# Kernel optimization log

Measured on AMD Instinct MI355X. Metric: run time of the kernel, lower is better.

The kernel has to match this reference:

```python
import jax, jax.numpy as jnp
import numpy as np

B, T, E = 16, 1024, 1024
G, N, D = 4, 8, 128
V = 2048


def setup_inputs() -> dict:
    key = jax.random.key(0)
    k1, k2, k3, k4 = jax.random.split(key, 4)
    x_emb = jax.random.normal(k1, (B, T, E), dtype=jnp.float32)
    W_in = jax.random.normal(k2, (E, G * N * D), dtype=jnp.float32) / np.sqrt(E)
    R = jax.random.normal(k3, (G, N, D, D), dtype=jnp.float32) / np.sqrt(D)
    b = jnp.zeros((G, N, D), dtype=jnp.float32)
    W_proj = jax.random.normal(k4, (V, N * D), dtype=jnp.float32) / np.sqrt(D)
    b_proj = jnp.zeros((V,), dtype=jnp.float32)
    return {"x_emb": x_emb, "W_in": W_in, "R": R, "b": b, "W_proj": W_proj, "b_proj": b_proj}


def reference(x_emb, W_in, R, b, W_proj, b_proj):
    # Input projection for all timesteps at once: [B,T,G,N,D]
    Bx, Tx, Ex = x_emb.shape
    Wx = jnp.einsum('bte,eg->btg', x_emb, W_in).reshape(Bx, Tx, G, N, D)

    def step(carry, wx_t):
        h, c = carry  # [B,N,D] each
        # per-head matrix recurrence: R[g] @ h  -> [B,G,N,D]
        gates = wx_t + jnp.einsum('gnde,bne->bgnd', R, h) + b
        i = jax.nn.sigmoid(gates[:, 0])
        f = jax.nn.sigmoid(gates[:, 1])
        z = jnp.tanh(gates[:, 2])
        o = jax.nn.sigmoid(gates[:, 3])
        c_new = f * c + i * z
        h_new = o * jnp.tanh(c_new)
        return (h_new, c_new), h_new

    h0 = jnp.zeros((Bx, N, D), dtype=x_emb.dtype)
    c0 = jnp.zeros((Bx, N, D), dtype=x_emb.dtype)
    (hN, cN), hs = jax.lax.scan(step, (h0, c0), jnp.swapaxes(Wx, 0, 1))  # hs: [T,B,N,D]
    h_flat = jnp.swapaxes(hs, 0, 1).reshape(Bx, Tx, N * D)
    logits = jnp.einsum('btn,vn->btv', h_flat, W_proj) + b_proj
    return logits
```

## Files before the change

### kernel.cpp

```cpp
#include <hip/hip_runtime.h>
#include <hip/hip_bf16.h>

#define DEV __device__ __forceinline__

using bf16 = __hip_bfloat16;
typedef __attribute__((ext_vector_type(8))) short short8v;
typedef __attribute__((ext_vector_type(4))) float f32x4;

constexpr int Bq = 16, Tq = 1024, Eq = 1024, Gq = 4, Nq = 8, Dq = 128, Vq = 2048;
constexpr int M1 = Bq * Tq;
constexpr int N1q = Gq * Nq * Dq;
constexpr int K1 = Eq;
constexpr int K2 = Nq * Dq;
constexpr int N2 = Vq;

DEV unsigned short bfu(float x) {
  union { bf16 h; unsigned short u; } cv;
  cv.h = __float2bfloat16(x);
  return cv.u;
}

DEV float rcp_(float x) { return __builtin_amdgcn_rcpf(x); }
DEV float sigm(float x) { return rcp_(1.0f + __expf(-x)); }
DEV float tanh_(float x) { return fmaf(2.0f, rcp_(1.0f + __expf(-2.0f * x)), -1.0f); }

#define GLD16(gp, lp)                                                       \
  __builtin_amdgcn_global_load_lds(                                        \
      (const __attribute__((address_space(1))) void*)(gp),                 \
      (__attribute__((address_space(3))) void*)(lp), 16, 0, 0)

#define SBAR0() __builtin_amdgcn_sched_barrier(0)
#define RAWBAR()                                                            \
  do { SBAR0(); __builtin_amdgcn_s_barrier(); SBAR0(); } while (0)
#define VMW6() asm volatile("s_waitcnt vmcnt(6)" ::: "memory")
#define VMW3() asm volatile("s_waitcnt vmcnt(3)" ::: "memory")
#define VMW0() asm volatile("s_waitcnt vmcnt(0)" ::: "memory")

__global__ __launch_bounds__(256) void cast_f32_bf16(const float* __restrict__ s,
                                                     bf16* __restrict__ d, int n4) {
  const int i = blockIdx.x * 256 + threadIdx.x;
  if (i >= n4) return;
  const float4 v = ((const float4*)s)[i];
  ushort4 u;
  u.x = bfu(v.x); u.y = bfu(v.y); u.z = bfu(v.z); u.w = bfu(v.w);
  ((ushort4*)d)[i] = u;
}

__global__ __launch_bounds__(256) void transpose_cast_perm(const float* __restrict__ s,
                                                           bf16* __restrict__ d,
                                                           int SK, int SN) {
  __shared__ float t[32][33];
  const int n0 = blockIdx.x * 32, k0 = blockIdx.y * 32;
  const int tx = threadIdx.x & 31, ty = threadIdx.x >> 5;
#pragma unroll
  for (int i = 0; i < 32; i += 8)
    t[ty + i][tx] = s[(size_t)(k0 + ty + i) * SN + n0 + tx];
  __syncthreads();
#pragma unroll
  for (int i = 0; i < 32; i += 8) {
    const int c = n0 + ty + i;
    const int g = c >> 10, n = (c >> 7) & 7, dd = c & 127;
    const int rp = n * 512 + dd * 4 + g;
    d[(size_t)rp * SK + k0 + tx] = __float2bfloat16(t[tx][ty + i]);
  }
}

__global__ __launch_bounds__(256) void zero_flags(unsigned int* __restrict__ f) {
  f[blockIdx.x * 256 + threadIdx.x] = 0u;
}

__global__ __launch_bounds__(256) void gemm_out(const bf16* __restrict__ A,
                                                const bf16* __restrict__ Bt,
                                                float* __restrict__ C,
                                                const float* __restrict__ bp,
                                                int K, int N) {
  __shared__ bf16 As[128 * 32];
  __shared__ bf16 Bs[128 * 32];
  const int m0 = blockIdx.y * 128, n0 = blockIdx.x * 128;
  const int tid = threadIdx.x;
  const int lane = tid & 63, w = tid >> 6;
  const int wm = w >> 1, wn = w & 1;

  const int srow = lane >> 2, scol = (lane & 3) * 8;
  const int ca = w * 2;
  const bf16* Ag0 = A + (size_t)(m0 + ca * 16 + srow) * K + scol;
  const bf16* Ag1 = Ag0 + (size_t)16 * K;
  const bf16* Bg0 = Bt + (size_t)(n0 + ca * 16 + srow) * K + scol;
  const bf16* Bg1 = Bg0 + (size_t)16 * K;
  bf16* Al0 = As + ca * 512;
  bf16* Al1 = Al0 + 512;
  bf16* Bl0 = Bs + ca * 512;
  bf16* Bl1 = Bl0 + 512;

  f32x4 acc[4][4] = {};
  const int rr = lane & 15;
  const int kb = (lane >> 4) * 8;

  for (int k0 = 0; k0 < K; k0 += 32) {
    GLD16(Ag0 + k0, Al0);
    GLD16(Ag1 + k0, Al1);
    GLD16(Bg0 + k0, Bl0);
    GLD16(Bg1 + k0, Bl1);
    __syncthreads();
    short8v af[4], bfr[4];
#pragma unroll
    for (int i = 0; i < 4; ++i) {
      af[i]  = *(const short8v*)&As[(wm * 64 + i * 16 + rr) * 32 + kb];
      bfr[i] = *(const short8v*)&Bs[(wn * 64 + i * 16 + rr) * 32 + kb];
    }
#pragma unroll
    for (int i = 0; i < 4; ++i)
#pragma unroll
      for (int j = 0; j < 4; ++j)
        acc[i][j] = __builtin_amdgcn_mfma_f32_16x16x32_bf16(af[i], bfr[j], acc[i][j], 0, 0, 0);
    __syncthreads();
  }

  const int crow = (lane >> 4) * 4, ccol = lane & 15;
  float bv[4];
#pragma unroll
  for (int j = 0; j < 4; ++j) bv[j] = bp[n0 + wn * 64 + j * 16 + ccol];
#pragma unroll
  for (int i = 0; i < 4; ++i)
#pragma unroll
    for (int j = 0; j < 4; ++j) {
      const size_t base =
          (size_t)(m0 + wm * 64 + i * 16 + crow) * N + (n0 + wn * 64 + j * 16 + ccol);
#pragma unroll
      for (int jj = 0; jj < 4; ++jj)
        C[base + (size_t)jj * N] = acc[i][j][jj] + bv[j];
    }
}

__global__ __launch_bounds__(512) void fused_xw_lstm(
    const bf16* __restrict__ xb, const bf16* __restrict__ WiT,
    bf16* __restrict__ Wx, const float* __restrict__ bp,
    const float* __restrict__ R, bf16* __restrict__ h_all,
    unsigned int* flags) {
  __shared__ bf16 Ab[4][128 * 32];
  __shared__ bf16 Bb[4][2][128 * 32];
  __shared__ __align__(16) unsigned short hl[2][4][144];

  const int bid = blockIdx.x;
  const int tid = threadIdx.x;

  if (bid < 224) {
    const int lane = tid & 63;
    const int w8 = tid >> 6;
    const int ts = w8 >> 2;
    const int w4 = w8 & 3;
    const int wm = w4 >> 1, wn = w4 & 1;
    const int rr = lane & 15, kb = (lane >> 4) * 8;
    const int crow = (lane >> 4) * 4, ccol = lane & 15;
    const int frow = 16 * w8 + (lane >> 2);
    const int fcol = (lane & 3) * 8;
    bf16* const Adst = &Ab[0][16 * w8 * 32];
    bf16* const B0dst = &Bb[0][0][16 * w8 * 32];
    bf16* const B1dst = &Bb[0][1][16 * w8 * 32];

    for (int pi = bid; pi < 2048; pi += 224) {
      const int tix0 = pi * 2;
      const int s = tix0 >> 9;
      const int rem = tix0 & 511;
      const int bn = rem >> 2, q0 = rem & 3;
      const int b = bn >> 3, n = bn & 7;
      const int m0 = (b * 8 + s) * 128;
      const int n0base = (n * 4 + q0) * 128;

      const bf16* Asrc = xb + (size_t)(m0 + frow) * 1024 + fcol;
      const bf16* B0src = WiT + (size_t)(n0base + frow) * 1024 + fcol;
      const bf16* B1src = B0src + (size_t)128 * 1024;

#define FILLCHUNK(BUF, KC)                                                   \
  do {                                                                       \
    const size_t go_ = (size_t)(KC) * 32;                                    \
    GLD16(Asrc + go_, Adst + (BUF) * 4096);                                  \
    GLD16(B0src + go_, B0dst + (BUF) * 8192);                                \
    GLD16(B1src + go_, B1dst + (BUF) * 8192);                                \
  } while (0)

      f32x4 acc[4][4] = {};

#define COMPUTECHUNK(BUF)                                                    \
  do {                                                                       \
    const bf16* Ap_ = &Ab[(BUF)][0];                                         \
    const bf16* Bp_ = &Bb[(BUF)][ts][0];                                     \
    short8v af[4], bfr[4];                                                   \
    _Pragma("unroll") for (int i2 = 0; i2 < 4; ++i2) {                       \
      af[i2]  = *(const short8v*)&Ap_[(wm * 64 + i2 * 16 + rr) * 32 + kb];   \
      bfr[i2] = *(const short8v*)&Bp_[(wn * 64 + i2 * 16 + rr) * 32 + kb];   \
    }                                                                        \
    _Pragma("unroll") for (int i2 = 0; i2 < 4; ++i2)                         \
      _Pragma("unroll") for (int j2 = 0; j2 < 4; ++j2)                       \
        acc[i2][j2] = __builtin_amdgcn_mfma_f32_16x16x32_bf16(               \
            af[i2], bfr[j2], acc[i2][j2], 0, 0, 0);                          \
  } while (0)

      FILLCHUNK(0, 0);
      FILLCHUNK(1, 1);
      for (int i = 0; i < 30; ++i) {
        FILLCHUNK((i + 2) & 3, i + 2);
        VMW6();
        RAWBAR();
        COMPUTECHUNK(i & 3);
      }
      VMW3();
      RAWBAR();
      COMPUTECHUNK(2);
      VMW0();
      RAWBAR();
      COMPUTECHUNK(3);

      {
        const int n0t = n0base + ts * 128;
#pragma unroll
        for (int i = 0; i < 4; ++i)
#pragma unroll
          for (int j = 0; j < 4; ++j) {
            const int pc = n0t + wn * 64 + j * 16 + ccol;
            const int nn = pc >> 9, gd = pc & 511;
            const int g = gd & 3, dd = gd >> 2;
            const float bvj = bp[(g * 8 + nn) * 128 + dd];
#pragma unroll
            for (int jj = 0; jj < 4; ++jj) {
              const int row = m0 + wm * 64 + i * 16 + crow + jj;
              const int bb = row >> 10, t = row & 1023;
              const size_t idx = (((size_t)(bb * 8 + nn) << 10) + t) * 512 + gd;
              Wx[idx] = __float2bfloat16(acc[i][j][jj] + bvj);
            }
          }
      }
      __syncthreads();
      if (tid == 0) {
        __threadfence();
        __hip_atomic_fetch_add(&flags[bn * 8 + s], 2u,
                               __ATOMIC_RELEASE, __HIP_MEMORY_SCOPE_AGENT);
      }
    }
#undef FILLCHUNK
#undef COMPUTECHUNK
  } else {
    const int cid = bid - 224;
    const int n = cid & 7, bq = cid >> 3;
    const int w = tid >> 6, lane = tid & 63;
    const int lg = lane >> 4, lc = lane & 15;
    const int bloc = lc & 3;
    const int ci = lc >> 2;
    const int dsite = 16 * w + 4 * ci + lg;

    short8v Af[4][4];
#pragma unroll
    for (int tau = 0; tau < 4; ++tau) {
      const int gd = 64 * w + 16 * tau + lc;
      const int g = gd & 3, d = gd >> 2;
      const float* rbase = R + ((size_t)(g * 8 + n) * 128 + d) * 128;
#pragma unroll
      for (int kf = 0; kf < 4; ++kf) {
        const float* rp = rbase + 32 * kf + 8 * lg;
        const float4 r0 = *(const float4*)rp;
        const float4 r1 = *(const float4*)(rp + 4);
        short8v bv;
        bv[0] = (short)bfu(r0.x); bv[1] = (short)bfu(r0.y);
        bv[2] = (short)bfu(r0.z); bv[3] = (short)bfu(r0.w);
        bv[4] = (short)bfu(r1.x); bv[5] = (short)bfu(r1.y);
        bv[6] = (short)bfu(r1.z); bv[7] = (short)bfu(r1.w);
        Af[tau][kf] = bv;
      }
    }

    for (int i = tid; i < 4 * 144; i += 512) (&hl[0][0][0])[i] = 0;
    __syncthreads();

    const bf16* wxb =
        Wx + ((size_t)((bq * 4 + bloc) * 8 + n) << 10) * 512 + dsite * 4;
    bf16* hout = h_all + ((size_t)(bq * 4 + bloc) << 20) + n * 128 + dsite;

    float c = 0.f;

    for (int s = 0; s < 8; ++s) {
      if (tid == 0) {
#pragma unroll
        for (int j = 0; j < 4; ++j) {
          const int fidx = ((bq * 4 + j) * 8 + n) * 8 + s;
          while (__hip_atomic_load(&flags[fidx], __ATOMIC_RELAXED,
                                   __HIP_MEMORY_SCOPE_AGENT) < 4u)
            __builtin_amdgcn_s_sleep(2);
        }
        __threadfence();
      }
      __syncthreads();

      ushort4 wxr[4];
#pragma unroll
      for (int u = 0; u < 4; ++u)
        wxr[u] = *(const ushort4*)(wxb + (size_t)(s * 128 + u) * 512);

      const int tend = s * 128 + 128;
      for (int t0 = s * 128; t0 < tend; t0 += 4) {
#pragma unroll
        for (int u = 0; u < 4; ++u) {
          const int t = t0 + u;
          const unsigned short* hb = &hl[t & 1][0][0];
          short8v Bf[4];
#pragma unroll
          for (int kf = 0; kf < 4; ++kf)
            Bf[kf] = *(const short8v*)(hb + bloc * 144 + kf * 32 + lg * 8);

          const ushort4 wxc = wxr[u];

          f32x4 acc[4];
#pragma unroll
          for (int tau = 0; tau < 4; ++tau) {
            acc[tau][0] = 0.f; acc[tau][1] = 0.f;
            acc[tau][2] = 0.f; acc[tau][3] = 0.f;
          }
#pragma unroll
          for (int kf = 0; kf < 4; ++kf)
#pragma unroll
            for (int tau = 0; tau < 4; ++tau)
              acc[tau] = __builtin_amdgcn_mfma_f32_16x16x32_bf16(
                  Af[tau][kf], Bf[kf], acc[tau], 0, 0, 0);

          {
            const int tp = (t + 4 < tend) ? (t + 4) : (tend - 1);
            wxr[u] = *(const ushort4*)(wxb + (size_t)tp * 512);
          }

          float pre0 = (ci & 2) ? ((ci & 1) ? acc[3][0] : acc[2][0])
                                : ((ci & 1) ? acc[1][0] : acc[0][0]);
          float pre1 = (ci & 2) ? ((ci & 1) ? acc[3][1] : acc[2][1])
                                : ((ci & 1) ? acc[1][1] : acc[0][1]);
          float pre2 = (ci & 2) ? ((ci & 1) ? acc[3][2] : acc[2][2])
                                : ((ci & 1) ? acc[1][2] : acc[0][2]);
          float pre3 = (ci & 2) ? ((ci & 1) ? acc[3][3] : acc[2][3])
                                : ((ci & 1) ? acc[1][3] : acc[0][3]);
          pre0 += __uint_as_float((unsigned)wxc.x << 16);
          pre1 += __uint_as_float((unsigned)wxc.y << 16);
          pre2 += __uint_as_float((unsigned)wxc.z << 16);
          pre3 += __uint_as_float((unsigned)wxc.w << 16);

          const float i_ = sigm(pre0);
          const float f_ = sigm(pre1);
          const float z_ = tanh_(pre2);
          const float o_ = sigm(pre3);
          c = f_ * c + i_ * z_;
          const float h = o_ * tanh_(c);
          const bf16 h16 = __float2bfloat16(h);

          hl[(t + 1) & 1][bloc][dsite] = ((const unsigned short*)&h16)[0];
          hout[(size_t)t << 10] = h16;

          __builtin_amdgcn_sched_barrier(0);
          asm volatile("s_waitcnt lgkmcnt(0)" ::: "memory");
          __builtin_amdgcn_sched_barrier(0);
          __builtin_amdgcn_s_barrier();
          __builtin_amdgcn_sched_barrier(0);
        }
      }
    }
  }
}

extern "C" void kernel_launch(void* const* d_in, const int* in_sizes, int n_in,
                              void* d_out, int out_size, void* d_ws, size_t ws_size,
                              hipStream_t stream) {
  const float* x_emb = (const float*)d_in[0];
  const float* W_in  = (const float*)d_in[1];
  const float* R     = (const float*)d_in[2];
  const float* bias  = (const float*)d_in[3];
  const float* W_prj = (const float*)d_in[4];
  const float* b_prj = (const float*)d_in[5];

  char* ws = (char*)d_ws;
  bf16* xb  = (bf16*)ws;
  bf16* WiT = (bf16*)(ws + (size_t)M1 * K1 * 2);
  bf16* Wpb = WiT + (size_t)N1q * K1;
  bf16* H   = Wpb + (size_t)N2 * K2;
  unsigned int* flags = (unsigned int*)(ws + ((size_t)76 << 20));
  bf16* Wx = (bf16*)d_out;

  cast_f32_bf16<<<(M1 * K1 / 4 + 255) / 256, 256, 0, stream>>>(x_emb, xb, M1 * K1 / 4);
  transpose_cast_perm<<<dim3(N1q / 32, K1 / 32), 256, 0, stream>>>(W_in, WiT, K1, N1q);
  cast_f32_bf16<<<(N2 * K2 / 4 + 255) / 256, 256, 0, stream>>>(W_prj, Wpb, N2 * K2 / 4);
  zero_flags<<<4, 256, 0, stream>>>(flags);

  fused_xw_lstm<<<dim3(256), dim3(512), 0, stream>>>(xb, WiT, Wx, bias, R, H, flags);

  gemm_out<<<dim3(N2 / 128, M1 / 128), 256, 0, stream>>>(
      H, Wpb, (float*)d_out, b_prj, K2, N2);
}
```

Baseline: 767.8 us.

## Fuse output projection into persistent LSTM kernel with per-chunk h flags

Moves the final vocabulary projection GEMM into the persistent fused kernel. The 224 GEMM blocks, once they finish the input projection, wait on new per-(batch, time-chunk) flags that the recurrence blocks publish. They then compute logits tiles while the serial recurrence keeps running. The Wx scratch in the output buffer is re-laid out so each (batch, chunk) slice lines up with the logits rows that later overwrite it, which keeps the in-place reuse safe. The cost is a second launch traded for spin-waiting. The projection GEMM now uses only 224 blocks with a smaller 128x128 tile per 8-wave block, so it may run below full-device throughput after the recurrence ends.

Result: slower. 793.9 us (+3.4%).

```diff
diff --git a/kernel.cpp b/kernel.cpp
--- a/kernel.cpp
+++ b/kernel.cpp
@@ -69,74 +69,12 @@
   f[blockIdx.x * 256 + threadIdx.x] = 0u;
 }
 
-__global__ __launch_bounds__(256) void gemm_out(const bf16* __restrict__ A,
-                                                const bf16* __restrict__ Bt,
-                                                float* __restrict__ C,
-                                                const float* __restrict__ bp,
-                                                int K, int N) {
-  __shared__ bf16 As[128 * 32];
-  __shared__ bf16 Bs[128 * 32];
-  const int m0 = blockIdx.y * 128, n0 = blockIdx.x * 128;
-  const int tid = threadIdx.x;
-  const int lane = tid & 63, w = tid >> 6;
-  const int wm = w >> 1, wn = w & 1;
-
-  const int srow = lane >> 2, scol = (lane & 3) * 8;
-  const int ca = w * 2;
-  const bf16* Ag0 = A + (size_t)(m0 + ca * 16 + srow) * K + scol;
-  const bf16* Ag1 = Ag0 + (size_t)16 * K;
-  const bf16* Bg0 = Bt + (size_t)(n0 + ca * 16 + srow) * K + scol;
-  const bf16* Bg1 = Bg0 + (size_t)16 * K;
-  bf16* Al0 = As + ca * 512;
-  bf16* Al1 = Al0 + 512;
-  bf16* Bl0 = Bs + ca * 512;
-  bf16* Bl1 = Bl0 + 512;
-
-  f32x4 acc[4][4] = {};
-  const int rr = lane & 15;
-  const int kb = (lane >> 4) * 8;
-
-  for (int k0 = 0; k0 < K; k0 += 32) {
-    GLD16(Ag0 + k0, Al0);
-    GLD16(Ag1 + k0, Al1);
-    GLD16(Bg0 + k0, Bl0);
-    GLD16(Bg1 + k0, Bl1);
-    __syncthreads();
-    short8v af[4], bfr[4];
-#pragma unroll
-    for (int i = 0; i < 4; ++i) {
-      af[i]  = *(const short8v*)&As[(wm * 64 + i * 16 + rr) * 32 + kb];
-      bfr[i] = *(const short8v*)&Bs[(wn * 64 + i * 16 + rr) * 32 + kb];
-    }
-#pragma unroll
-    for (int i = 0; i < 4; ++i)
-#pragma unroll
-      for (int j = 0; j < 4; ++j)
-        acc[i][j] = __builtin_amdgcn_mfma_f32_16x16x32_bf16(af[i], bfr[j], acc[i][j], 0, 0, 0);
-    __syncthreads();
-  }
-
-  const int crow = (lane >> 4) * 4, ccol = lane & 15;
-  float bv[4];
-#pragma unroll
-  for (int j = 0; j < 4; ++j) bv[j] = bp[n0 + wn * 64 + j * 16 + ccol];
-#pragma unroll
-  for (int i = 0; i < 4; ++i)
-#pragma unroll
-    for (int j = 0; j < 4; ++j) {
-      const size_t base =
-          (size_t)(m0 + wm * 64 + i * 16 + crow) * N + (n0 + wn * 64 + j * 16 + ccol);
-#pragma unroll
-      for (int jj = 0; jj < 4; ++jj)
-        C[base + (size_t)jj * N] = acc[i][j][jj] + bv[j];
-    }
-}
-
-__global__ __launch_bounds__(512) void fused_xw_lstm(
+__global__ __launch_bounds__(512) void fused_all(
     const bf16* __restrict__ xb, const bf16* __restrict__ WiT,
-    bf16* __restrict__ Wx, const float* __restrict__ bp,
+    bf16* __restrict__ WxC, const float* __restrict__ bp,
     const float* __restrict__ R, bf16* __restrict__ h_all,
-    unsigned int* flags) {
+    const bf16* __restrict__ Wpb, const float* __restrict__ bprj,
+    float* __restrict__ out, unsigned int* wxflags, unsigned int* hflags) {
   __shared__ bf16 Ab[4][128 * 32];
   __shared__ bf16 Bb[4][2][128 * 32];
   __shared__ __align__(16) unsigned short hl[2][4][144];
@@ -147,29 +85,30 @@
   if (bid < 224) {
     const int lane = tid & 63;
     const int w8 = tid >> 6;
-    const int ts = w8 >> 2;
-    const int w4 = w8 & 3;
-    const int wm = w4 >> 1, wn = w4 & 1;
-    const int rr = lane & 15, kb = (lane >> 4) * 8;
-    const int crow = (lane >> 4) * 4, ccol = lane & 15;
-    const int frow = 16 * w8 + (lane >> 2);
-    const int fcol = (lane & 3) * 8;
-    bf16* const Adst = &Ab[0][16 * w8 * 32];
-    bf16* const B0dst = &Bb[0][0][16 * w8 * 32];
-    bf16* const B1dst = &Bb[0][1][16 * w8 * 32];
-
-    for (int pi = bid; pi < 2048; pi += 224) {
-      const int tix0 = pi * 2;
-      const int s = tix0 >> 9;
-      const int rem = tix0 & 511;
-      const int bn = rem >> 2, q0 = rem & 3;
-      const int b = bn >> 3, n = bn & 7;
-      const int m0 = (b * 8 + s) * 128;
-      const int n0base = (n * 4 + q0) * 128;
-
-      const bf16* Asrc = xb + (size_t)(m0 + frow) * 1024 + fcol;
-      const bf16* B0src = WiT + (size_t)(n0base + frow) * 1024 + fcol;
-      const bf16* B1src = B0src + (size_t)128 * 1024;
+    {
+      const int ts = w8 >> 2;
+      const int w4 = w8 & 3;
+      const int wm = w4 >> 1, wn = w4 & 1;
+      const int rr = lane & 15, kb = (lane >> 4) * 8;
+      const int crow = (lane >> 4) * 4, ccol = lane & 15;
+      const int frow = 16 * w8 + (lane >> 2);
+      const int fcol = (lane & 3) * 8;
+      bf16* const Adst = &Ab[0][16 * w8 * 32];
+      bf16* const B0dst = &Bb[0][0][16 * w8 * 32];
+      bf16* const B1dst = &Bb[0][1][16 * w8 * 32];
+
+      for (int pi = bid; pi < 2048; pi += 224) {
+        const int tix0 = pi * 2;
+        const int s = tix0 >> 9;
+        const int rem = tix0 & 511;
+        const int bn = rem >> 2, q0 = rem & 3;
+        const int b = bn >> 3, n = bn & 7;
+        const int m0 = (b * 8 + s) * 128;
+        const int n0base = (n * 4 + q0) * 128;
+
+        const bf16* Asrc = xb + (size_t)(m0 + frow) * 1024 + fcol;
+        const bf16* B0src = WiT + (size_t)(n0base + frow) * 1024 + fcol;
+        const bf16* B1src = B0src + (size_t)128 * 1024;
 
 #define FILLCHUNK(BUF, KC)                                                   \
   do {                                                                       \
@@ -179,7 +118,7 @@
     GLD16(B1src + go_, B1dst + (BUF) * 8192);                                \
   } while (0)
 
-      f32x4 acc[4][4] = {};
+        f32x4 acc[4][4] = {};
 
 #define COMPUTECHUNK(BUF)                                                    \
   do {                                                                       \
@@ -196,49 +135,114 @@
             af[i2], bfr[j2], acc[i2][j2], 0, 0, 0);                          \
   } while (0)
 
-      FILLCHUNK(0, 0);
-      FILLCHUNK(1, 1);
-      for (int i = 0; i < 30; ++i) {
-        FILLCHUNK((i + 2) & 3, i + 2);
-        VMW6();
+        FILLCHUNK(0, 0);
+        FILLCHUNK(1, 1);
+        for (int i = 0; i < 30; ++i) {
+          FILLCHUNK((i + 2) & 3, i + 2);
+          VMW6();
+          RAWBAR();
+          COMPUTECHUNK(i & 3);
+        }
+        VMW3();
         RAWBAR();
-        COMPUTECHUNK(i & 3);
-      }
-      VMW3();
-      RAWBAR();
-      COMPUTECHUNK(2);
-      VMW0();
-      RAWBAR();
-      COMPUTECHUNK(3);
-
-      {
-        const int n0t = n0base + ts * 128;
-#pragma unroll
-        for (int i = 0; i < 4; ++i)
-#pragma unroll
-          for (int j = 0; j < 4; ++j) {
-            const int pc = n0t + wn * 64 + j * 16 + ccol;
-            const int nn = pc >> 9, gd = pc & 511;
-            const int g = gd & 3, dd = gd >> 2;
-            const float bvj = bp[(g * 8 + nn) * 128 + dd];
-#pragma unroll
-            for (int jj = 0; jj < 4; ++jj) {
-              const int row = m0 + wm * 64 + i * 16 + crow + jj;
-              const int bb = row >> 10, t = row & 1023;
-              const size_t idx = (((size_t)(bb * 8 + nn) << 10) + t) * 512 + gd;
-              Wx[idx] = __float2bfloat16(acc[i][j][jj] + bvj);
+        COMPUTECHUNK(2);
+        VMW0();
+        RAWBAR();
+        COMPUTECHUNK(3);
+
+        {
+          const int n0t = n0base + ts * 128;
+#pragma unroll
+          for (int i = 0; i < 4; ++i)
+#pragma unroll
+            for (int j = 0; j < 4; ++j) {
+              const int pc = n0t + wn * 64 + j * 16 + ccol;
+              const int nn = pc >> 9, gd = pc & 511;
+              const int g = gd & 3, dd = gd >> 2;
+              const float bvj = bp[(g * 8 + nn) * 128 + dd];
+#pragma unroll
+              for (int jj = 0; jj < 4; ++jj) {
+                const int row = m0 + wm * 64 + i * 16 + crow + jj;
+                const int bb = row >> 10, ss = (row >> 7) & 7, tau = row & 127;
+                const size_t idx = ((size_t)bb << 22) + ((size_t)ss << 19) +
+                                   ((size_t)(nn * 128 + tau) << 9) + gd;
+                WxC[idx] = __float2bfloat16(acc[i][j][jj] + bvj);
+              }
             }
-          }
-      }
-      __syncthreads();
-      if (tid == 0) {
-        __threadfence();
-        __hip_atomic_fetch_add(&flags[bn * 8 + s], 2u,
-                               __ATOMIC_RELEASE, __HIP_MEMORY_SCOPE_AGENT);
-      }
-    }
+        }
+        __syncthreads();
+        if (tid == 0) {
+          __threadfence();
+          __hip_atomic_fetch_add(&wxflags[bn * 8 + s], 2u,
+                                 __ATOMIC_RELEASE, __HIP_MEMORY_SCOPE_AGENT);
+        }
+      }
 #undef FILLCHUNK
 #undef COMPUTECHUNK
+    }
+    {
+      bf16* const AsO = &Ab[0][0];
+      bf16* const BsO = &Ab[1][0];
+      const int wm2 = w8 >> 2, wn2 = w8 & 3;
+      const int srow = lane >> 2, scol = (lane & 3) * 8;
+      const int rr = lane & 15, kb = (lane >> 4) * 8;
+      const int crow = (lane >> 4) * 4, ccol = lane & 15;
+      __syncthreads();
+
+      for (int oi = bid; oi < 2048; oi += 224) {
+        const int so = oi >> 8;
+        const int rem = oi & 255;
+        const int bo = rem >> 4, nc = rem & 15;
+        const int m0 = bo * 1024 + so * 128;
+        const int n0 = nc * 128;
+
+        if (tid == 0) {
+          while (__hip_atomic_load(&hflags[bo * 8 + so], __ATOMIC_RELAXED,
+                                   __HIP_MEMORY_SCOPE_AGENT) < 8u)
+            __builtin_amdgcn_s_sleep(16);
+          __threadfence();
+        }
+        __syncthreads();
+
+        f32x4 acc[4][2] = {};
+        const bf16* Ag = h_all + (size_t)(m0 + 16 * w8 + srow) * 1024 + scol;
+        const bf16* Bg = Wpb + (size_t)(n0 + 16 * w8 + srow) * 1024 + scol;
+        for (int k0 = 0; k0 < 1024; k0 += 32) {
+          GLD16(Ag + k0, AsO + w8 * 512);
+          GLD16(Bg + k0, BsO + w8 * 512);
+          __syncthreads();
+          short8v af[4], bfr[2];
+#pragma unroll
+          for (int i = 0; i < 4; ++i)
+            af[i] = *(const short8v*)&AsO[(wm2 * 64 + i * 16 + rr) * 32 + kb];
+#pragma unroll
+          for (int j = 0; j < 2; ++j)
+            bfr[j] = *(const short8v*)&BsO[(wn2 * 32 + j * 16 + rr) * 32 + kb];
+#pragma unroll
+          for (int i = 0; i < 4; ++i)
+#pragma unroll
+            for (int j = 0; j < 2; ++j)
+              acc[i][j] = __builtin_amdgcn_mfma_f32_16x16x32_bf16(
+                  af[i], bfr[j], acc[i][j], 0, 0, 0);
+          __syncthreads();
+        }
+        float bv[2];
+#pragma unroll
+        for (int j = 0; j < 2; ++j) bv[j] = bprj[n0 + wn2 * 32 + j * 16 + ccol];
+#pragma unroll
+        for (int i = 0; i < 4; ++i)
+#pragma unroll
+          for (int j = 0; j < 2; ++j) {
+            const size_t base =
+                (size_t)(m0 + wm2 * 64 + i * 16 + crow) * N2 +
+                (n0 + wn2 * 32 + j * 16 + ccol);
+#pragma unroll
+            for (int jj = 0; jj < 4; ++jj)
+              out[base + (size_t)jj * N2] = acc[i][j][jj] + bv[j];
+          }
+        __syncthreads();
+      }
+    }
   } else {
     const int cid = bid - 224;
     const int n = cid & 7, bq = cid >> 3;
@@ -247,6 +251,7 @@
     const int bloc = lc & 3;
     const int ci = lc >> 2;
     const int dsite = 16 * w + 4 * ci + lg;
+    const int b = bq * 4 + bloc;
 
     short8v Af[4][4];
 #pragma unroll
@@ -271,10 +276,7 @@
     for (int i = tid; i < 4 * 144; i += 512) (&hl[0][0][0])[i] = 0;
     __syncthreads();
 
-    const bf16* wxb =
-        Wx + ((size_t)((bq * 4 + bloc) * 8 + n) << 10) * 512 + dsite * 4;
-    bf16* hout = h_all + ((size_t)(bq * 4 + bloc) << 20) + n * 128 + dsite;
-
+    bf16* hout = h_all + ((size_t)b << 20) + n * 128 + dsite;
     float c = 0.f;
 
     for (int s = 0; s < 8; ++s) {
@@ -282,7 +284,7 @@
 #pragma unroll
         for (int j = 0; j < 4; ++j) {
           const int fidx = ((bq * 4 + j) * 8 + n) * 8 + s;
-          while (__hip_atomic_load(&flags[fidx], __ATOMIC_RELAXED,
+          while (__hip_atomic_load(&wxflags[fidx], __ATOMIC_RELAXED,
                                    __HIP_MEMORY_SCOPE_AGENT) < 4u)
             __builtin_amdgcn_s_sleep(2);
         }
@@ -290,16 +292,19 @@
       }
       __syncthreads();
 
+      const bf16* wxs = WxC + ((size_t)b << 22) + ((size_t)s << 19) +
+                        ((size_t)(n * 128) << 9) + dsite * 4;
+
       ushort4 wxr[4];
 #pragma unroll
       for (int u = 0; u < 4; ++u)
-        wxr[u] = *(const ushort4*)(wxb + (size_t)(s * 128 + u) * 512);
-
-      const int tend = s * 128 + 128;
-      for (int t0 = s * 128; t0 < tend; t0 += 4) {
+        wxr[u] = *(const ushort4*)(wxs + (size_t)u * 512);
+
+      for (int tau0 = 0; tau0 < 128; tau0 += 4) {
 #pragma unroll
         for (int u = 0; u < 4; ++u) {
-          const int t = t0 + u;
+          const int tau = tau0 + u;
+          const int t = s * 128 + tau;
           const unsigned short* hb = &hl[t & 1][0][0];
           short8v Bf[4];
 #pragma unroll
@@ -310,20 +315,20 @@
 
           f32x4 acc[4];
 #pragma unroll
-          for (int tau = 0; tau < 4; ++tau) {
-            acc[tau][0] = 0.f; acc[tau][1] = 0.f;
-            acc[tau][2] = 0.f; acc[tau][3] = 0.f;
+          for (int tt = 0; tt < 4; ++tt) {
+            acc[tt][0] = 0.f; acc[tt][1] = 0.f;
+            acc[tt][2] = 0.f; acc[tt][3] = 0.f;
           }
 #pragma unroll
           for (int kf = 0; kf < 4; ++kf)
 #pragma unroll
-            for (int tau = 0; tau < 4; ++tau)
-              acc[tau] = __builtin_amdgcn_mfma_f32_16x16x32_bf16(
-                  Af[tau][kf], Bf[kf], acc[tau], 0, 0, 0);
+            for (int tt = 0; tt < 4; ++tt)
+              acc[tt] = __builtin_amdgcn_mfma_f32_16x16x32_bf16(
+                  Af[tt][kf], Bf[kf], acc[tt], 0, 0, 0);
 
           {
-            const int tp = (t + 4 < tend) ? (t + 4) : (tend - 1);
-            wxr[u] = *(const ushort4*)(wxb + (size_t)tp * 512);
+            const int tp = (tau + 4 < 128) ? (tau + 4) : 127;
+            wxr[u] = *(const ushort4*)(wxs + (size_t)tp * 512);
           }
 
           float pre0 = (ci & 2) ? ((ci & 1) ? acc[3][0] : acc[2][0])
@@ -357,6 +362,15 @@
           __builtin_amdgcn_sched_barrier(0);
         }
       }
+
+      __syncthreads();
+      if (tid == 0) {
+        __threadfence();
+#pragma unroll
+        for (int j = 0; j < 4; ++j)
+          __hip_atomic_fetch_add(&hflags[(bq * 4 + j) * 8 + s], 1u,
+                                 __ATOMIC_RELEASE, __HIP_MEMORY_SCOPE_AGENT);
+      }
     }
   }
 }
@@ -377,15 +391,15 @@
   bf16* Wpb = WiT + (size_t)N1q * K1;
   bf16* H   = Wpb + (size_t)N2 * K2;
   unsigned int* flags = (unsigned int*)(ws + ((size_t)76 << 20));
+  unsigned int* wxflags = flags;
+  unsigned int* hflags  = flags + 1024;
   bf16* Wx = (bf16*)d_out;
 
   cast_f32_bf16<<<(M1 * K1 / 4 + 255) / 256, 256, 0, stream>>>(x_emb, xb, M1 * K1 / 4);
   transpose_cast_perm<<<dim3(N1q / 32, K1 / 32), 256, 0, stream>>>(W_in, WiT, K1, N1q);
   cast_f32_bf16<<<(N2 * K2 / 4 + 255) / 256, 256, 0, stream>>>(W_prj, Wpb, N2 * K2 / 4);
-  zero_flags<<<4, 256, 0, stream>>>(flags);
-
-  fused_xw_lstm<<<dim3(256), dim3(512), 0, stream>>>(xb, WiT, Wx, bias, R, H, flags);
-
-  gemm_out<<<dim3(N2 / 128, M1 / 128), 256, 0, stream>>>(
-      H, Wpb, (float*)d_out, b_prj, K2, N2);
-}
+  zero_flags<<<5, 256, 0, stream>>>(flags);
+
+  fused_all<<<dim3(256), dim3(512), 0, stream>>>(
+      xb, WiT, Wx, bias, R, H, Wpb, b_prj, (float*)d_out, wxflags, hflags);
+}
```
